# Kernel optimization log

Measured on AMD Instinct MI355X. Metric: run time of the kernel, lower is better.

The kernel has to match this reference:

```python
import jax, jax.numpy as jnp
import numpy as np

D_MODEL = 1024
HIDDEN = 2048
D_STATE = 16
KERN = 3
BATCH = 2
SEQ = 2048


def _layernorm(x, g, b, eps=1e-5):
    m = jnp.mean(x, axis=-1, keepdims=True)
    v = jnp.var(x, axis=-1, keepdims=True)
    return (x - m) * jax.lax.rsqrt(v + eps) * g + b


def setup_inputs() -> dict:
    key = jax.random.key(0)
    ks = jax.random.split(key, 10)
    w_scale = 0.02  # keep pre-activations in a sane range (mimics trained-net init)
    return {
        "x": jax.random.normal(ks[0], (BATCH, SEQ, D_MODEL), jnp.float32),
        "W_x": jax.random.normal(ks[1], (HIDDEN, D_MODEL), jnp.float32) * w_scale,
        "b_x": jnp.zeros((HIDDEN,), jnp.float32),
        "W_g": jax.random.normal(ks[2], (HIDDEN, D_MODEL), jnp.float32) * w_scale,
        "b_g": jnp.zeros((HIDDEN,), jnp.float32),
        "conv_w": jax.random.normal(ks[3], (HIDDEN, 1, KERN), jnp.float32) * 0.3,
        "conv_b": jnp.zeros((HIDDEN,), jnp.float32),
        "A_raw": jax.random.normal(ks[4], (HIDDEN, D_STATE), jnp.float32),
        "B_ssm": jax.random.normal(ks[5], (HIDDEN, D_STATE), jnp.float32),
        "C_ssm": jax.random.normal(ks[6], (HIDDEN, D_STATE), jnp.float32),
        "W_dt": jax.random.normal(ks[7], (HIDDEN, D_MODEL), jnp.float32) * w_scale,
        "b_dt": jnp.zeros((HIDDEN,), jnp.float32),
        "W_out": jax.random.normal(ks[8], (D_MODEL, HIDDEN), jnp.float32) * w_scale,
        "b_out": jnp.zeros((D_MODEL,), jnp.float32),
        "ln_g": jnp.ones((D_MODEL,), jnp.float32),
        "ln_b": jnp.zeros((D_MODEL,), jnp.float32),
    }


def reference(x, W_x, b_x, W_g, b_g, conv_w, conv_b, A_raw, B_ssm, C_ssm,
              W_dt, b_dt, W_out, b_out, ln_g, ln_b):
    # projections: u, gate
    u = jnp.einsum('bld,hd->blh', x, W_x) + b_x                    # [B,L,H]
    g = jax.nn.sigmoid(jnp.einsum('bld,hd->blh', x, W_g) + b_g)    # [B,L,H]
    # depthwise conv over time (padding = kernel//2, 'same' for odd kernel)
    pad = conv_w.shape[-1] // 2
    h = jax.lax.conv_general_dilated(
        jnp.transpose(u, (0, 2, 1)), conv_w,
        window_strides=(1,), padding=[(pad, pad)],
        feature_group_count=conv_w.shape[0],
        dimension_numbers=('NCH', 'OIH', 'NCH')) + conv_b[None, :, None]
    h = jnp.transpose(h, (0, 2, 1))                                # [B,L,H]
    u = u * g + h * (1.0 - g)
    # time-invariant dt per channel (mean over batch & time, clamped)
    dt = jax.nn.softplus(jnp.einsum('bld,hd->blh', x, W_dt) + b_dt).mean(axis=(0, 1))
    dt = jnp.clip(dt, 1e-3, 2.0)                                   # [H]
    # discretize
    A = -jax.nn.softplus(A_raw)                                    # [H,S]
    A_d = jnp.exp(A * dt[:, None])                                 # [H,S]
    B_d = (A_d - 1.0) / (A + 1e-6) * B_ssm                         # [H,S]
    # selective scan: state s[b,h,k] = A_d*s + B_d*u_t ; y = <s, C>
    Bsz, L, H = u.shape
    S = A_d.shape[1]

    def step(carry, u_t):                                          # u_t: [B,H]
        new = A_d[None] * carry + B_d[None] * u_t[:, :, None]      # [B,H,S]
        y_t = jnp.einsum('bhs,hs->bh', new, C_ssm)
        return new, y_t

    init = jnp.zeros((Bsz, H, S), dtype=u.dtype)
    _, ys = jax.lax.scan(step, init, jnp.transpose(u, (1, 0, 2)))  # ys: [L,B,H]
    y = jnp.transpose(ys, (1, 0, 2))                               # [B,L,H]
    out = jnp.einsum('blh,dh->bld', y, W_out) + b_out
    return _layernorm(x + out, ln_g, ln_b)
```

## Files before the change

### kernel.cpp

```cpp
#include <hip/hip_runtime.h>
#include <math.h>

#define D_MODEL 1024
#define HIDDEN  2048
#define D_STATE 16
#define BATCH   2
#define SEQ     2048
#define NTOK    (BATCH*SEQ)
#define CHUNK   64
#define NCHUNK  (SEQ/CHUNK)

typedef __attribute__((ext_vector_type(8))) short bf16x8;
typedef __attribute__((ext_vector_type(4))) float f32x4;

#define GLOAD_LDS16(gptr, lptr) \
    __builtin_amdgcn_global_load_lds((const __attribute__((address_space(1))) void*)(gptr), \
                                     (__attribute__((address_space(3))) void*)(lptr), 16, 0, 0)

__device__ __forceinline__ float softplus_f(float x) {
    return fmaxf(x, 0.0f) + log1pf(expf(-fabsf(x)));
}
__device__ __forceinline__ float sigmoid_f(float x) {
    return 1.0f / (1.0f + expf(-x));
}
__device__ __forceinline__ ushort f2bf(float f) {
    unsigned u = __float_as_uint(f);
    unsigned r = (u + 0x7fffu + ((u >> 16) & 1u)) >> 16;
    return (ushort)r;
}
__device__ __forceinline__ float bf2f(ushort u) {
    return __uint_as_float(((unsigned)u) << 16);
}

__global__ __launch_bounds__(256) void cvt_all(
    const float* __restrict__ x, const float* __restrict__ Wx,
    const float* __restrict__ Wg, const float* __restrict__ Wdt,
    const float* __restrict__ Wout, ushort* __restrict__ arena)
{
    int i = blockIdx.x * 256 + threadIdx.x;
    const float* src; int base;
    if      (i < 1048576) { src = x;    base = 0; }
    else if (i < 1572864) { src = Wx;   base = 1048576; }
    else if (i < 2097152) { src = Wg;   base = 1572864; }
    else if (i < 2621440) { src = Wdt;  base = 2097152; }
    else                  { src = Wout; base = 2621440; }
    float4 v = reinterpret_cast<const float4*>(src)[i - base];
    ushort4 o = { f2bf(v.x), f2bf(v.y), f2bf(v.z), f2bf(v.w) };
    reinterpret_cast<ushort4*>(arena)[i] = o;
}

__device__ __forceinline__ void kloop_128(
    const ushort* __restrict__ A, const ushort* __restrict__ B,
    int K, int m0, int n0, ushort* As, ushort* Bs,
    f32x4 (&acc)[4][4], int lane, int w, int wm, int wn)
{
    const int lr   = lane >> 2;
    const int p    = lane & 3;
    const int quad = lane >> 4;
    const int fr   = lane & 15;
    for (int k0 = 0; k0 < K; k0 += 32) {
        #pragma unroll
        for (int j = 0; j < 2; j++) {
            const int slab = w * 2 + j;
            const int r    = slab * 16 + lr;
            const int q    = (p - (r >> 2)) & 3;
            const ushort* ga = A + (size_t)(m0 + r) * K + k0 + q * 8;
            const ushort* gb = B + (size_t)(n0 + r) * K + k0 + q * 8;
            GLOAD_LDS16(ga, &As[slab * 512]);
            GLOAD_LDS16(gb, &Bs[slab * 512]);
        }
        __syncthreads();
        bf16x8 af[4], bfv[4];
        #pragma unroll
        for (int t = 0; t < 4; t++) {
            int ra = wm * 64 + t * 16 + fr;
            int pa = (quad + (ra >> 2)) & 3;
            af[t]  = *reinterpret_cast<const bf16x8*>(&As[ra * 32 + pa * 8]);
            int rb = wn * 64 + t * 16 + fr;
            int pb = (quad + (rb >> 2)) & 3;
            bfv[t] = *reinterpret_cast<const bf16x8*>(&Bs[rb * 32 + pb * 8]);
        }
        #pragma unroll
        for (int i = 0; i < 4; i++)
            #pragma unroll
            for (int j = 0; j < 4; j++)
                acc[i][j] = __builtin_amdgcn_mfma_f32_16x16x32_bf16(af[i], bfv[j], acc[i][j], 0, 0, 0);
        __syncthreads();
    }
}

__global__ __launch_bounds__(256) void proj_gemm_fused(
    const ushort* __restrict__ xbf, const ushort* __restrict__ Wcat,
    const float* __restrict__ b_x, const float* __restrict__ b_g,
    const float* __restrict__ b_dt, ushort* __restrict__ u_out,
    ushort* __restrict__ g_out, float* __restrict__ dt_sum)
{
    __shared__ ushort As[128 * 32];
    __shared__ ushort Bs[128 * 32];
    const int tid = threadIdx.x, lane = tid & 63, w = tid >> 6;
    const int wm = w & 1, wn = w >> 1;
    const int m0 = blockIdx.y * 128, n0 = blockIdx.x * 128;
    const int quad = lane >> 4, fr = lane & 15;

    f32x4 acc[4][4];
    #pragma unroll
    for (int i = 0; i < 4; i++)
        #pragma unroll
        for (int j = 0; j < 4; j++)
            acc[i][j] = (f32x4){0.f, 0.f, 0.f, 0.f};

    kloop_128(xbf, Wcat, D_MODEL, m0, n0, As, Bs, acc, lane, w, wm, wn);

    const int region = n0 >> 11;
    const int nc0 = (n0 & 2047) + wn * 64;

    if (region == 2) {
        #pragma unroll
        for (int j = 0; j < 4; j++) {
            int n = nc0 + j * 16 + fr;
            float bj = b_dt[n];
            float s = 0.f;
            #pragma unroll
            for (int i = 0; i < 4; i++)
                #pragma unroll
                for (int r = 0; r < 4; r++)
                    s += softplus_f(acc[i][j][r] + bj);
            s += __shfl_xor(s, 16);
            s += __shfl_xor(s, 32);
            if (lane < 16) atomicAdd(&dt_sum[n], s);
        }
    } else {
        const float* bias = region ? b_g : b_x;
        ushort* out = region ? g_out : u_out;
        #pragma unroll
        for (int j = 0; j < 4; j++) {
            int n = nc0 + j * 16 + fr;
            float bj = bias[n];
            #pragma unroll
            for (int i = 0; i < 4; i++) {
                int mrow = m0 + wm * 64 + i * 16 + quad * 4;
                #pragma unroll
                for (int r = 0; r < 4; r++) {
                    float v = acc[i][j][r] + bj;
                    if (region) v = sigmoid_f(v);
                    out[(size_t)(mrow + r) * HIDDEN + n] = f2bf(v);
                }
            }
        }
    }
}

__global__ __launch_bounds__(256) void gemm_out(
    const ushort* __restrict__ ybf, const ushort* __restrict__ Wout,
    const float* __restrict__ b_out, const float* __restrict__ x,
    float* __restrict__ resid)
{
    __shared__ ushort As[128 * 32];
    __shared__ ushort Bs[128 * 32];
    const int tid = threadIdx.x, lane = tid & 63, w = tid >> 6;
    const int wm = w & 1, wn = w >> 1;
    const int m0 = blockIdx.y * 128, n0 = blockIdx.x * 128;
    const int quad = lane >> 4, fr = lane & 15;

    f32x4 acc[4][4];
    #pragma unroll
    for (int i = 0; i < 4; i++)
        #pragma unroll
        for (int j = 0; j < 4; j++)
            acc[i][j] = (f32x4){0.f, 0.f, 0.f, 0.f};

    kloop_128(ybf, Wout, HIDDEN, m0, n0, As, Bs, acc, lane, w, wm, wn);

    #pragma unroll
    for (int j = 0; j < 4; j++) {
        int n = n0 + wn * 64 + j * 16 + fr;
        float bj = b_out[n];
        #pragma unroll
        for (int i = 0; i < 4; i++) {
            int mrow = m0 + wm * 64 + i * 16 + quad * 4;
            #pragma unroll
            for (int r = 0; r < 4; r++) {
                size_t off = (size_t)(mrow + r) * D_MODEL + n;
                resid[off] = acc[i][j][r] + bj + x[off];
            }
        }
    }
}

__global__ __launch_bounds__(256) void dt_finalize(
    const float* __restrict__ dt_sum, const float* __restrict__ A_raw,
    const float* __restrict__ B_ssm, float* __restrict__ A_d,
    float* __restrict__ B_d, float* __restrict__ A_dL)
{
    int i = blockIdx.x * 256 + threadIdx.x;
    if (i >= HIDDEN * D_STATE) return;
    int h = i >> 4;
    float dt = dt_sum[h] * (1.0f / NTOK);
    dt = fminf(fmaxf(dt, 1e-3f), 2.0f);
    float Av = -softplus_f(A_raw[i]);
    float Ad = expf(Av * dt);
    float Bd = (Ad - 1.0f) / (Av + 1e-6f) * B_ssm[i];
    A_d[i] = Ad;
    B_d[i] = Bd;
    A_dL[i] = expf(Av * dt * CHUNK);
}

__global__ __launch_bounds__(256) void scan_pass1(
    const ushort* __restrict__ u_bf, const ushort* __restrict__ g_bf,
    const float* __restrict__ conv_w, const float* __restrict__ conv_b,
    const float* __restrict__ A_d, const float* __restrict__ B_d,
    const float* __restrict__ C_ssm,
    float* __restrict__ ypart, float* __restrict__ states)
{
    int idx = blockIdx.x * 256 + threadIdx.x;
    int h  = idx & (HIDDEN - 1);
    int bc = idx >> 11;
    int c  = bc & (NCHUNK - 1);
    int b  = bc >> 5;
    float Ad[D_STATE], Bd[D_STATE], Cv[D_STATE], st[D_STATE];
    const float4* a4 = reinterpret_cast<const float4*>(A_d  + h * D_STATE);
    const float4* b4 = reinterpret_cast<const float4*>(B_d  + h * D_STATE);
    const float4* c4 = reinterpret_cast<const float4*>(C_ssm + h * D_STATE);
    #pragma unroll
    for (int q = 0; q < 4; q++) {
        float4 av = a4[q], bv = b4[q], cv = c4[q];
        Ad[q*4+0]=av.x; Ad[q*4+1]=av.y; Ad[q*4+2]=av.z; Ad[q*4+3]=av.w;
        Bd[q*4+0]=bv.x; Bd[q*4+1]=bv.y; Bd[q*4+2]=bv.z; Bd[q*4+3]=bv.w;
        Cv[q*4+0]=cv.x; Cv[q*4+1]=cv.y; Cv[q*4+2]=cv.z; Cv[q*4+3]=cv.w;
    }
    #pragma unroll
    for (int s = 0; s < D_STATE; s++) st[s] = 0.f;

    float w0 = conv_w[h * 3 + 0], w1 = conv_w[h * 3 + 1];
    float w2 = conv_w[h * 3 + 2], cb = conv_b[h];
    const int tok0 = c * CHUNK;
    const size_t base = ((size_t)b * SEQ + tok0) * HIDDEN + h;
    float u_prev = (tok0 > 0) ? bf2f(u_bf[base - HIDDEN]) : 0.f;
    float u_cur  = bf2f(u_bf[base]);
    for (int l = 0; l < CHUNK; l++) {
        float u_next = (tok0 + l + 1 < SEQ) ? bf2f(u_bf[base + (size_t)(l + 1) * HIDDEN]) : 0.f;
        float gv = bf2f(g_bf[base + (size_t)l * HIDDEN]);
        float conv = u_prev * w0 + u_cur * w1 + u_next * w2 + cb;
        float uv = u_cur * gv + conv * (1.0f - gv);
        float yv = 0.f;
        #pragma unroll
        for (int s = 0; s < D_STATE; s++) {
            st[s] = fmaf(Ad[s], st[s], Bd[s] * uv);
            yv = fmaf(st[s], Cv[s], yv);
        }
        ypart[base + (size_t)l * HIDDEN] = yv;
        u_prev = u_cur; u_cur = u_next;
    }
    float4* sp = reinterpret_cast<float4*>(states + ((size_t)bc * HIDDEN + h) * D_STATE);
    #pragma unroll
    for (int q = 0; q < 4; q++)
        sp[q] = (float4){st[q*4+0], st[q*4+1], st[q*4+2], st[q*4+3]};
}

__global__ __launch_bounds__(256) void scan_pass2(
    float* __restrict__ states, const float* __restrict__ A_dL)
{
    int idx = blockIdx.x * 256 + threadIdx.x;
    int s = idx & 15;
    int h = (idx >> 4) & (HIDDEN - 1);
    int b = idx >> 15;
    float aL = A_dL[h * D_STATE + s];
    float carry = 0.f;
    for (int c = 0; c < NCHUNK; c++) {
        size_t addr = (((size_t)(b * NCHUNK + c) * HIDDEN) + h) * D_STATE + s;
        float fin = states[addr];
        states[addr] = carry;
        carry = fmaf(aL, carry, fin);
    }
}

__global__ __launch_bounds__(256) void scan_pass3(
    const float* __restrict__ ypart, const float* __restrict__ states,
    const float* __restrict__ A_d, const float* __restrict__ C_ssm,
    ushort* __restrict__ ybf)
{
    int idx = blockIdx.x * 256 + threadIdx.x;
    int h  = idx & (HIDDEN - 1);
    int bc = idx >> 11;
    int c  = bc & (NCHUNK - 1);
    int b  = bc >> 5;
    float Ad[D_STATE], t[D_STATE];
    const float* sp = states + ((size_t)bc * HIDDEN + h) * D_STATE;
    #pragma unroll
    for (int s = 0; s < D_STATE; s++) {
        float a = A_d[h * D_STATE + s];
        Ad[s] = a;
        t[s] = C_ssm[h * D_STATE + s] * a * sp[s];
    }
    const size_t base = ((size_t)b * SEQ + (size_t)c * CHUNK) * HIDDEN + h;
    for (int l = 0; l < CHUNK; l++) {
        float corr = 0.f;
        #pragma unroll
        for (int s = 0; s < D_STATE; s++) {
            corr += t[s];
            t[s] *= Ad[s];
        }
        ybf[base + (size_t)l * HIDDEN] = f2bf(ypart[base + (size_t)l * HIDDEN] + corr);
    }
}

__global__ __launch_bounds__(256) void ln_kernel(
    const float* __restrict__ resid, const float* __restrict__ ln_g,
    const float* __restrict__ ln_b, float* __restrict__ out)
{
    int row = blockIdx.x;
    int tid = threadIdx.x;
    const float4 v = reinterpret_cast<const float4*>(resid + (size_t)row * D_MODEL)[tid];
    float s  = v.x + v.y + v.z + v.w;
    float ss = v.x * v.x + v.y * v.y + v.z * v.z + v.w * v.w;
    #pragma unroll
    for (int off = 32; off > 0; off >>= 1) {
        s  += __shfl_down(s, off);
        ss += __shfl_down(ss, off);
    }
    __shared__ float sbuf[4], ssbuf[4];
    int wid = tid >> 6, lane = tid & 63;
    if (lane == 0) { sbuf[wid] = s; ssbuf[wid] = ss; }
    __syncthreads();
    float tot  = sbuf[0] + sbuf[1] + sbuf[2] + sbuf[3];
    float tot2 = ssbuf[0] + ssbuf[1] + ssbuf[2] + ssbuf[3];
    float mean = tot * (1.0f / D_MODEL);
    float var  = tot2 * (1.0f / D_MODEL) - mean * mean;
    float rstd = rsqrtf(var + 1e-5f);
    const float4 gv = reinterpret_cast<const float4*>(ln_g)[tid];
    const float4 bv = reinterpret_cast<const float4*>(ln_b)[tid];
    float4 o;
    o.x = (v.x - mean) * rstd * gv.x + bv.x;
    o.y = (v.y - mean) * rstd * gv.y + bv.y;
    o.z = (v.z - mean) * rstd * gv.z + bv.z;
    o.w = (v.w - mean) * rstd * gv.w + bv.w;
    reinterpret_cast<float4*>(out + (size_t)row * D_MODEL)[tid] = o;
}

extern "C" void kernel_launch(void* const* d_in, const int* in_sizes, int n_in,
                              void* d_out, int out_size, void* d_ws, size_t ws_size,
                              hipStream_t stream) {
    const float* x      = (const float*)d_in[0];
    const float* W_x    = (const float*)d_in[1];
    const float* b_x    = (const float*)d_in[2];
    const float* W_g    = (const float*)d_in[3];
    const float* b_g    = (const float*)d_in[4];
    const float* conv_w = (const float*)d_in[5];
    const float* conv_b = (const float*)d_in[6];
    const float* A_raw  = (const float*)d_in[7];
    const float* B_ssm  = (const float*)d_in[8];
    const float* C_ssm  = (const float*)d_in[9];
    const float* W_dt   = (const float*)d_in[10];
    const float* b_dt   = (const float*)d_in[11];
    const float* W_out  = (const float*)d_in[12];
    const float* b_out  = (const float*)d_in[13];
    const float* ln_g   = (const float*)d_in[14];
    const float* ln_b   = (const float*)d_in[15];

    char* W = (char*)d_ws;
    ushort* arena   = (ushort*)(W);
    ushort* x_bf    = arena;
    ushort* Wcat    = arena + 4194304;
    ushort* Wout_bf = arena + 10485760;
    ushort* u_bf    = (ushort*)(W + (24ull << 20));
    ushort* g_bf    = (ushort*)(W + (40ull << 20));
    float*  ypart   = (float*)(W + (56ull << 20));
    float*  states  = (float*)(W + (88ull << 20));
    float*  dt_sum  = (float*)(W + (96ull << 20));
    float*  A_d     = (float*)(W + (96ull << 20) + 65536);
    float*  B_d     = (float*)(W + (96ull << 20) + 65536 + 131072);
    float*  A_dL    = (float*)(W + (96ull << 20) + 65536 + 262144);
    ushort* y_bf    = u_bf;
    float*  resid   = ypart;

    hipMemsetAsync(dt_sum, 0, HIDDEN * sizeof(float), stream);

    dim3 blk(256);
    cvt_all<<<12288, blk, 0, stream>>>(x, W_x, W_g, W_dt, W_out, arena);

    dim3 grid_proj(3 * HIDDEN / 128, NTOK / 128);
    proj_gemm_fused<<<grid_proj, blk, 0, stream>>>(x_bf, Wcat, b_x, b_g, b_dt,
                                                   u_bf, g_bf, dt_sum);
    dt_finalize<<<(HIDDEN * D_STATE) / 256, blk, 0, stream>>>(dt_sum, A_raw, B_ssm,
                                                              A_d, B_d, A_dL);
    scan_pass1<<<(BATCH * NCHUNK * HIDDEN) / 256, blk, 0, stream>>>(
        u_bf, g_bf, conv_w, conv_b, A_d, B_d, C_ssm, ypart, states);
    scan_pass2<<<(BATCH * HIDDEN * D_STATE) / 256, blk, 0, stream>>>(states, A_dL);
    scan_pass3<<<(BATCH * NCHUNK * HIDDEN) / 256, blk, 0, stream>>>(ypart, states, A_d,
                                                                    C_ssm, y_bf);
    dim3 grid_out(D_MODEL / 128, NTOK / 128);
    gemm_out<<<grid_out, blk, 0, stream>>>(y_bf, Wout_bf, b_out, x, resid);
    ln_kernel<<<NTOK, blk, 0, stream>>>(resid, ln_g, ln_b, (float*)d_out);
}
```

Measured before the change: 350.7 us.

## Double-buffer GEMM LDS tiles, drop swizzle, store scan partials as bf16

The GEMM k-loop now double-buffers its LDS tiles. The next K-slab's global-to-LDS loads are issued right after a single barrier and before the current slab's MFMAs, which overlaps load latency with compute and removes one barrier per iteration. The LDS XOR swizzle is dropped, which may add bank conflicts, and launch bounds request 5 waves per SIMD. Separately, the scan's intra-chunk partial outputs are stored as bf16 instead of fp32, halving that intermediate's traffic at some precision cost. The workspace layout is adjusted to match.

```diff
diff --git a/kernel.cpp b/kernel.cpp
--- a/kernel.cpp
+++ b/kernel.cpp
@@ -49,54 +49,64 @@
     reinterpret_cast<ushort4*>(arena)[i] = o;
 }
 
-__device__ __forceinline__ void kloop_128(
+__device__ __forceinline__ void kloop_dbuf(
     const ushort* __restrict__ A, const ushort* __restrict__ B,
     int K, int m0, int n0, ushort* As, ushort* Bs,
     f32x4 (&acc)[4][4], int lane, int w, int wm, int wn)
 {
     const int lr   = lane >> 2;
-    const int p    = lane & 3;
+    const int kc   = (lane & 3) * 8;
     const int quad = lane >> 4;
     const int fr   = lane & 15;
+
+    const int slab0 = w * 2;
+    const int r0 = slab0 * 16 + lr;
+    const int r1 = r0 + 16;
+    const size_t ga0 = (size_t)(m0 + r0) * K + kc;
+    const size_t ga1 = (size_t)(m0 + r1) * K + kc;
+    const size_t gb0 = (size_t)(n0 + r0) * K + kc;
+    const size_t gb1 = (size_t)(n0 + r1) * K + kc;
+
+    GLOAD_LDS16(A + ga0, &As[slab0 * 512]);
+    GLOAD_LDS16(A + ga1, &As[slab0 * 512 + 512]);
+    GLOAD_LDS16(B + gb0, &Bs[slab0 * 512]);
+    GLOAD_LDS16(B + gb1, &Bs[slab0 * 512 + 512]);
+
+    int buf = 0;
     for (int k0 = 0; k0 < K; k0 += 32) {
-        #pragma unroll
-        for (int j = 0; j < 2; j++) {
-            const int slab = w * 2 + j;
-            const int r    = slab * 16 + lr;
-            const int q    = (p - (r >> 2)) & 3;
-            const ushort* ga = A + (size_t)(m0 + r) * K + k0 + q * 8;
-            const ushort* gb = B + (size_t)(n0 + r) * K + k0 + q * 8;
-            GLOAD_LDS16(ga, &As[slab * 512]);
-            GLOAD_LDS16(gb, &Bs[slab * 512]);
-        }
         __syncthreads();
+        if (k0 + 32 < K) {
+            const int nb = (buf ^ 1) * 4096;
+            GLOAD_LDS16(A + ga0 + k0 + 32, &As[nb + slab0 * 512]);
+            GLOAD_LDS16(A + ga1 + k0 + 32, &As[nb + slab0 * 512 + 512]);
+            GLOAD_LDS16(B + gb0 + k0 + 32, &Bs[nb + slab0 * 512]);
+            GLOAD_LDS16(B + gb1 + k0 + 32, &Bs[nb + slab0 * 512 + 512]);
+        }
+        const ushort* as = &As[buf * 4096];
+        const ushort* bs = &Bs[buf * 4096];
         bf16x8 af[4], bfv[4];
         #pragma unroll
         for (int t = 0; t < 4; t++) {
-            int ra = wm * 64 + t * 16 + fr;
-            int pa = (quad + (ra >> 2)) & 3;
-            af[t]  = *reinterpret_cast<const bf16x8*>(&As[ra * 32 + pa * 8]);
-            int rb = wn * 64 + t * 16 + fr;
-            int pb = (quad + (rb >> 2)) & 3;
-            bfv[t] = *reinterpret_cast<const bf16x8*>(&Bs[rb * 32 + pb * 8]);
+            af[t]  = *reinterpret_cast<const bf16x8*>(&as[(wm * 64 + t * 16 + fr) * 32 + quad * 8]);
+            bfv[t] = *reinterpret_cast<const bf16x8*>(&bs[(wn * 64 + t * 16 + fr) * 32 + quad * 8]);
         }
         #pragma unroll
         for (int i = 0; i < 4; i++)
             #pragma unroll
             for (int j = 0; j < 4; j++)
                 acc[i][j] = __builtin_amdgcn_mfma_f32_16x16x32_bf16(af[i], bfv[j], acc[i][j], 0, 0, 0);
-        __syncthreads();
-    }
-}
-
-__global__ __launch_bounds__(256) void proj_gemm_fused(
+        buf ^= 1;
+    }
+}
+
+__global__ __launch_bounds__(256, 5) void proj_gemm_fused(
     const ushort* __restrict__ xbf, const ushort* __restrict__ Wcat,
     const float* __restrict__ b_x, const float* __restrict__ b_g,
     const float* __restrict__ b_dt, ushort* __restrict__ u_out,
     ushort* __restrict__ g_out, float* __restrict__ dt_sum)
 {
-    __shared__ ushort As[128 * 32];
-    __shared__ ushort Bs[128 * 32];
+    __shared__ ushort As[8192];
+    __shared__ ushort Bs[8192];
     const int tid = threadIdx.x, lane = tid & 63, w = tid >> 6;
     const int wm = w & 1, wn = w >> 1;
     const int m0 = blockIdx.y * 128, n0 = blockIdx.x * 128;
@@ -109,7 +119,7 @@
         for (int j = 0; j < 4; j++)
             acc[i][j] = (f32x4){0.f, 0.f, 0.f, 0.f};
 
-    kloop_128(xbf, Wcat, D_MODEL, m0, n0, As, Bs, acc, lane, w, wm, wn);
+    kloop_dbuf(xbf, Wcat, D_MODEL, m0, n0, As, Bs, acc, lane, w, wm, wn);
 
     const int region = n0 >> 11;
     const int nc0 = (n0 & 2047) + wn * 64;
@@ -150,13 +160,13 @@
     }
 }
 
-__global__ __launch_bounds__(256) void gemm_out(
+__global__ __launch_bounds__(256, 5) void gemm_out(
     const ushort* __restrict__ ybf, const ushort* __restrict__ Wout,
     const float* __restrict__ b_out, const float* __restrict__ x,
     float* __restrict__ resid)
 {
-    __shared__ ushort As[128 * 32];
-    __shared__ ushort Bs[128 * 32];
+    __shared__ ushort As[8192];
+    __shared__ ushort Bs[8192];
     const int tid = threadIdx.x, lane = tid & 63, w = tid >> 6;
     const int wm = w & 1, wn = w >> 1;
     const int m0 = blockIdx.y * 128, n0 = blockIdx.x * 128;
@@ -169,7 +179,7 @@
         for (int j = 0; j < 4; j++)
             acc[i][j] = (f32x4){0.f, 0.f, 0.f, 0.f};
 
-    kloop_128(ybf, Wout, HIDDEN, m0, n0, As, Bs, acc, lane, w, wm, wn);
+    kloop_dbuf(ybf, Wout, HIDDEN, m0, n0, As, Bs, acc, lane, w, wm, wn);
 
     #pragma unroll
     for (int j = 0; j < 4; j++) {
@@ -210,7 +220,7 @@
     const float* __restrict__ conv_w, const float* __restrict__ conv_b,
     const float* __restrict__ A_d, const float* __restrict__ B_d,
     const float* __restrict__ C_ssm,
-    float* __restrict__ ypart, float* __restrict__ states)
+    ushort* __restrict__ ypart, float* __restrict__ states)
 {
     int idx = blockIdx.x * 256 + threadIdx.x;
     int h  = idx & (HIDDEN - 1);
@@ -248,7 +258,7 @@
             st[s] = fmaf(Ad[s], st[s], Bd[s] * uv);
             yv = fmaf(st[s], Cv[s], yv);
         }
-        ypart[base + (size_t)l * HIDDEN] = yv;
+        ypart[base + (size_t)l * HIDDEN] = f2bf(yv);
         u_prev = u_cur; u_cur = u_next;
     }
     float4* sp = reinterpret_cast<float4*>(states + ((size_t)bc * HIDDEN + h) * D_STATE);
@@ -275,7 +285,7 @@
 }
 
 __global__ __launch_bounds__(256) void scan_pass3(
-    const float* __restrict__ ypart, const float* __restrict__ states,
+    const ushort* __restrict__ ypart, const float* __restrict__ states,
     const float* __restrict__ A_d, const float* __restrict__ C_ssm,
     ushort* __restrict__ ybf)
 {
@@ -300,7 +310,7 @@
             corr += t[s];
             t[s] *= Ad[s];
         }
-        ybf[base + (size_t)l * HIDDEN] = f2bf(ypart[base + (size_t)l * HIDDEN] + corr);
+        ybf[base + (size_t)l * HIDDEN] = f2bf(bf2f(ypart[base + (size_t)l * HIDDEN]) + corr);
     }
 }
 
@@ -364,14 +374,14 @@
     ushort* Wout_bf = arena + 10485760;
     ushort* u_bf    = (ushort*)(W + (24ull << 20));
     ushort* g_bf    = (ushort*)(W + (40ull << 20));
-    float*  ypart   = (float*)(W + (56ull << 20));
-    float*  states  = (float*)(W + (88ull << 20));
-    float*  dt_sum  = (float*)(W + (96ull << 20));
-    float*  A_d     = (float*)(W + (96ull << 20) + 65536);
-    float*  B_d     = (float*)(W + (96ull << 20) + 65536 + 131072);
-    float*  A_dL    = (float*)(W + (96ull << 20) + 65536 + 262144);
+    ushort* ypart   = (ushort*)(W + (56ull << 20));
+    float*  resid   = (float*)(W + (40ull << 20));
+    float*  states  = (float*)(W + (72ull << 20));
+    float*  dt_sum  = (float*)(W + (80ull << 20));
+    float*  A_d     = (float*)(W + (80ull << 20) + 65536);
+    float*  B_d     = (float*)(W + (80ull << 20) + 65536 + 131072);
+    float*  A_dL    = (float*)(W + (80ull << 20) + 65536 + 262144);
     ushort* y_bf    = u_bf;
-    float*  resid   = ypart;
 
     hipMemsetAsync(dt_sum, 0, HIDDEN * sizeof(float), stream);
 
```

After: 381.8 us. 8.9% more time.
